# Kernel optimization log

Measured on AMD Instinct MI355X. Metric: run time of the kernel, lower is better.

The kernel has to match this reference:

```python
import jax, jax.numpy as jnp
import numpy as np

N = 32        # fixed segment-tree span in the original module
LEVELS = 5    # log2(N) descent steps (l<r loop runs exactly 5 times)
B, S, D = 16, 8192, 64


def _prefix(x):
    # P[b, m] = sum_{l=1}^{m} x[b, l]  (leaf l holds x[l]; x[0] is never used)
    return jnp.concatenate([jnp.zeros_like(x[:, :1]), jnp.cumsum(x[:, 1:N], axis=1)], axis=1)


def _seg(P, a, b, n, bidx):
    # sum of leaves l in [a, b] with l < n, via prefix sums; shapes a,b,n: [B,S]
    hi = jnp.minimum(b, n - 1)
    ok = hi >= a
    hic = jnp.clip(hi, 0, N - 1)
    v = P[bidx, hic] - P[bidx, a - 1]          # [B,S,D]
    return jnp.where(ok[..., None], v, jnp.zeros((), P.dtype))


def reference(queries, keys, values, valid_lens):
    b, s, d = queries.shape
    if valid_lens is None:
        n = jnp.full((b, s), keys.shape[1], jnp.int32)
    elif valid_lens.ndim == 1:
        n = jnp.broadcast_to(valid_lens.astype(jnp.int32)[:, None], (b, s))
    else:
        n = valid_lens.astype(jnp.int32)
    Pk = _prefix(keys)    # [B,N,D]
    Pv = _prefix(values)  # [B,N,D]
    bidx = jnp.arange(b)[:, None]
    l = jnp.ones((b, s), jnp.int32)
    r = jnp.full((b, s), N, jnp.int32)
    ans = jnp.zeros((b, s, d), queries.dtype)
    for _ in range(LEVELS):
        mid = (l + r) >> 1
        kL = _seg(Pk, l, mid, n, bidx)
        kR = _seg(Pk, mid + 1, r, n, bidx)
        ls = jax.nn.sigmoid(jnp.sum(queries * kL, axis=-1))  # [B,S]
        rs = jax.nn.sigmoid(jnp.sum(queries * kR, axis=-1))
        cond = ls >= rs
        vL = _seg(Pv, l, mid, n, bidx)
        vR = _seg(Pv, mid + 1, r, n, bidx)
        add = jnp.where(cond[..., None], vR * rs[..., None], vL * ls[..., None])
        ans = ans * 0.5 + add
        r = jnp.where(cond, mid, r)
        l = jnp.where(cond, l, mid + 1)
    return ans


def setup_inputs() -> dict:
    key = jax.random.key(0)
    k1, k2, k3, k4 = jax.random.split(key, 4)
    return {
        "queries": jax.random.normal(k1, (B, S, D), jnp.float32),
        "keys": jax.random.normal(k2, (B, N, D), jnp.float32),
        "values": jax.random.normal(k3, (B, N, D), jnp.float32),
        "valid_lens": jax.random.randint(k4, (B,), 0, 32, jnp.int64),
    }
```

## Files before the change

kernel.cpp:

```cpp
#include <hip/hip_runtime.h>
#include <math.h>


#define SEG_N   32
#define DIM     64
#define LEVELS  5
#define QPB     64
#define THREADS 256
#define PAD     68

#define DPP_QUAD_XOR1   0xB1
#define DPP_QUAD_XOR2   0x4E
#define DPP_ROW_HMIRROR 0x141

template <int CTRL>
__device__ __forceinline__ float dpp_xadd(float v) {
    const int s = __builtin_amdgcn_update_dpp(0, __float_as_int(v), CTRL, 0xf, 0xf, true);
    return v + __int_as_float(s);
}

__device__ __forceinline__ float group8_sum(float v) {
    v = dpp_xadd<DPP_QUAD_XOR1>(v);
    v = dpp_xadd<DPP_QUAD_XOR2>(v);
    v = dpp_xadd<DPP_ROW_HMIRROR>(v);
    return v;
}

__device__ __forceinline__ float4 f4sub(const float4 a, const float4 b) {
    return make_float4(a.x - b.x, a.y - b.y, a.z - b.z, a.w - b.w);
}
__device__ __forceinline__ float4 sel4(bool c, const float4 a, const float4 b) {
    return make_float4(c ? a.x : b.x, c ? a.y : b.y, c ? a.z : b.z, c ? a.w : b.w);
}
__device__ __forceinline__ float dot4(const float4 a, const float4 b) {
    return a.x * b.x + a.y * b.y + a.z * b.z + a.w * b.w;
}
__device__ __forceinline__ void fma4(float4& acc, const float4 hi, const float4 lo, float w) {
    acc.x = fmaf(hi.x - lo.x, w, acc.x);
    acc.y = fmaf(hi.y - lo.y, w, acc.y);
    acc.z = fmaf(hi.z - lo.z, w, acc.z);
    acc.w = fmaf(hi.w - lo.w, w, acc.w);
}

__global__ __launch_bounds__(THREADS) void segtree_attn_kernel(
    const float* __restrict__ q,
    const float* __restrict__ keys,
    const float* __restrict__ values,
    const int*   __restrict__ vlen,
    float*       __restrict__ out,
    int S)
{
    __shared__ float Pk[SEG_N * PAD];
    __shared__ float Pv[SEG_N * PAD];

    const int b = blockIdx.y;
    const int t = threadIdx.x;
    const int g = t >> 3;
    const int u = t & 7;
    const int c = u * 8;

    const int sA = blockIdx.x * QPB + g;
    const int sB = sA + 32;

    const float* qpA = q + ((size_t)b * S + sA) * DIM + c;
    const float* qpB = q + ((size_t)b * S + sB) * DIM + c;
    const float4 qA0 = *(const float4*)qpA;
    const float4 qA1 = *(const float4*)(qpA + 4);
    const float4 qB0 = *(const float4*)qpB;
    const float4 qB1 = *(const float4*)(qpB + 4);

    if (t < 2 * DIM) {
        const int col = t & (DIM - 1);
        const float* src = ((t < DIM) ? keys : values) + (size_t)b * SEG_N * DIM + col;
        float* dst = (t < DIM) ? Pk : Pv;
        float acc = 0.0f;
        dst[col] = 0.0f;
        #pragma unroll
        for (int row = 1; row < SEG_N; ++row) {
            acc += src[row * DIM];
            dst[row * PAD + col] = acc;
        }
    }
    const int n = vlen[b];
    __syncthreads();

    const int hnc = max(min(n - 1, SEG_N - 1), 0);
    const float scale[LEVELS] = {0.0625f, 0.125f, 0.25f, 0.5f, 1.0f};

    const int cm16 = min(16, hnc);
    float4 pkM_A0 = *(const float4*)&Pk[cm16 * PAD + c];
    float4 pkM_A1 = *(const float4*)&Pk[cm16 * PAD + c + 4];
    float4 pkM_B0 = pkM_A0, pkM_B1 = pkM_A1;
    const float4 pkRi0 = *(const float4*)&Pk[hnc * PAD + c];
    const float4 pkRi1 = *(const float4*)&Pk[hnc * PAD + c + 4];

    float4 pkR_A0 = pkRi0, pkR_A1 = pkRi1;
    float4 pkR_B0 = pkRi0, pkR_B1 = pkRi1;
    float4 pkA_A0 = make_float4(0.f,0.f,0.f,0.f), pkA_A1 = make_float4(0.f,0.f,0.f,0.f);
    float4 pkA_B0 = make_float4(0.f,0.f,0.f,0.f), pkA_B1 = make_float4(0.f,0.f,0.f,0.f);

    int midA = 16, midB = 16;
    int lA = 1, rA = SEG_N, rowA_A = 0, rowR_A = hnc;
    int lB = 1, rB = SEG_N, rowA_B = 0, rowR_B = hnc;

    float wA[LEVELS], wB[LEVELS];
    int   rows[LEVELS];

    #pragma unroll
    for (int lev = 0; lev < LEVELS; ++lev) {
        const int step = 8 >> lev;
        const int cmA = min(midA, hnc);
        const int cmB = min(midB, hnc);

        float4 sLoA0, sLoA1, sHiA0, sHiA1, sLoB0, sLoB1, sHiB0, sHiB1;
        int midLoA = 0, midHiA = 0, midLoB = 0, midHiB = 0;
        if (lev < LEVELS - 1) {
            midLoA = midA - step; midHiA = midA + step;
            midLoB = midB - step; midHiB = midB + step;
            const int rLoA = min(midLoA, hnc), rHiA = min(midHiA, hnc);
            const int rLoB = min(midLoB, hnc), rHiB = min(midHiB, hnc);
            sLoA0 = *(const float4*)&Pk[rLoA * PAD + c];
            sLoA1 = *(const float4*)&Pk[rLoA * PAD + c + 4];
            sHiA0 = *(const float4*)&Pk[rHiA * PAD + c];
            sHiA1 = *(const float4*)&Pk[rHiA * PAD + c + 4];
            sLoB0 = *(const float4*)&Pk[rLoB * PAD + c];
            sLoB1 = *(const float4*)&Pk[rLoB * PAD + c + 4];
            sHiB0 = *(const float4*)&Pk[rHiB * PAD + c];
            sHiB1 = *(const float4*)&Pk[rHiB * PAD + c + 4];
        }

        float dLA = dot4(qA0, f4sub(pkM_A0, pkA_A0)) + dot4(qA1, f4sub(pkM_A1, pkA_A1));
        float dRA = dot4(qA0, f4sub(pkR_A0, pkM_A0)) + dot4(qA1, f4sub(pkR_A1, pkM_A1));
        float dLB = dot4(qB0, f4sub(pkM_B0, pkA_B0)) + dot4(qB1, f4sub(pkM_B1, pkA_B1));
        float dRB = dot4(qB0, f4sub(pkR_B0, pkM_B0)) + dot4(qB1, f4sub(pkR_B1, pkM_B1));

        dLA = group8_sum(dLA);
        dRA = group8_sum(dRA);
        dLB = group8_sum(dLB);
        dRB = group8_sum(dRB);

        const bool okLA = (min(midA, n - 1) >= lA);
        const bool okRA = (min(rA,   n - 1) >= midA + 1);
        const bool okLB = (min(midB, n - 1) >= lB);
        const bool okRB = (min(rB,   n - 1) >= midB + 1);

        const float sLA = okLA ? dLA : 0.0f;
        const float sRA = okRA ? dRA : 0.0f;
        const float sLB = okLB ? dLB : 0.0f;
        const float sRB = okRB ? dRB : 0.0f;

        const float lsA = 1.0f / (1.0f + __expf(-sLA));
        const float rsA = 1.0f / (1.0f + __expf(-sRA));
        const float lsB = 1.0f / (1.0f + __expf(-sLB));
        const float rsB = 1.0f / (1.0f + __expf(-sRB));

        const bool condA = (lsA >= rsA);
        const bool condB = (lsB >= rsB);

        const bool  okselA = condA ? okRA : okLA;
        const bool  okselB = condB ? okRB : okLB;
        const float wselA  = condA ? rsA : lsA;
        const float wselB  = condB ? rsB : lsB;
        wA[lev] = okselA ? (wselA * scale[lev]) : 0.0f;
        wB[lev] = okselB ? (wselB * scale[lev]) : 0.0f;

        const int hiA = condA ? rowR_A : cmA;
        const int loA = condA ? midA   : rowA_A;
        const int hiB = condB ? rowR_B : cmB;
        const int loB = condB ? midB   : rowA_B;
        rows[lev] = hiA | (loA << 8) | (hiB << 16) | (loB << 24);

        if (condA) {
            rA = midA; rowR_A = cmA;
            pkR_A0 = pkM_A0; pkR_A1 = pkM_A1;
        } else {
            lA = midA + 1; rowA_A = midA;
            pkA_A0 = pkM_A0; pkA_A1 = pkM_A1;
        }
        if (condB) {
            rB = midB; rowR_B = cmB;
            pkR_B0 = pkM_B0; pkR_B1 = pkM_B1;
        } else {
            lB = midB + 1; rowA_B = midB;
            pkA_B0 = pkM_B0; pkA_B1 = pkM_B1;
        }

        if (lev < LEVELS - 1) {
            midA = condA ? midLoA : midHiA;
            midB = condB ? midLoB : midHiB;
            pkM_A0 = sel4(condA, sLoA0, sHiA0);
            pkM_A1 = sel4(condA, sLoA1, sHiA1);
            pkM_B0 = sel4(condB, sLoB0, sHiB0);
            pkM_B1 = sel4(condB, sLoB1, sHiB1);
        }
    }

    float4 aA0 = make_float4(0.f,0.f,0.f,0.f), aA1 = make_float4(0.f,0.f,0.f,0.f);
    float4 aB0 = make_float4(0.f,0.f,0.f,0.f), aB1 = make_float4(0.f,0.f,0.f,0.f);
    #pragma unroll
    for (int lev = 0; lev < LEVELS; ++lev) {
        const int pk = rows[lev];
        const int hiAr = pk & 0xFF, loAr = (pk >> 8) & 0xFF;
        const int hiBr = (pk >> 16) & 0xFF, loBr = (pk >> 24) & 0xFF;
        const float4 hA0 = *(const float4*)&Pv[hiAr * PAD + c];
        const float4 hA1 = *(const float4*)&Pv[hiAr * PAD + c + 4];
        const float4 lA0 = *(const float4*)&Pv[loAr * PAD + c];
        const float4 lA1 = *(const float4*)&Pv[loAr * PAD + c + 4];
        fma4(aA0, hA0, lA0, wA[lev]);
        fma4(aA1, hA1, lA1, wA[lev]);
        const float4 hB0 = *(const float4*)&Pv[hiBr * PAD + c];
        const float4 hB1 = *(const float4*)&Pv[hiBr * PAD + c + 4];
        const float4 lB0 = *(const float4*)&Pv[loBr * PAD + c];
        const float4 lB1 = *(const float4*)&Pv[loBr * PAD + c + 4];
        fma4(aB0, hB0, lB0, wB[lev]);
        fma4(aB1, hB1, lB1, wB[lev]);
    }

    float* opA = out + ((size_t)b * S + sA) * DIM + c;
    float* opB = out + ((size_t)b * S + sB) * DIM + c;
    *(float4*)opA       = aA0;
    *(float4*)(opA + 4) = aA1;
    *(float4*)opB       = aB0;
    *(float4*)(opB + 4) = aB1;
}

extern "C" void kernel_launch(void* const* d_in, const int* in_sizes, int n_in,
                              void* d_out, int out_size, void* d_ws, size_t ws_size,
                              hipStream_t stream) {
    const float* q    = (const float*)d_in[0];
    const float* keys = (const float*)d_in[1];
    const float* vals = (const float*)d_in[2];
    const int*   vl   = (const int*)d_in[3];
    float* out = (float*)d_out;

    const int B = in_sizes[3];
    const int S = in_sizes[0] / (B * DIM);

    dim3 grid(S / QPB, B);
    segtree_attn_kernel<<<grid, THREADS, 0, stream>>>(q, keys, vals, vl, out, S);
}
```

Baseline: 26.81 us.

## Precompute prefix tables in a separate scan kernel and copy them into LDS

```diff
diff --git a/kernel.cpp b/kernel.cpp
--- a/kernel.cpp
+++ b/kernel.cpp
@@ -29,9 +29,6 @@
 __device__ __forceinline__ float4 f4sub(const float4 a, const float4 b) {
     return make_float4(a.x - b.x, a.y - b.y, a.z - b.z, a.w - b.w);
 }
-__device__ __forceinline__ float4 sel4(bool c, const float4 a, const float4 b) {
-    return make_float4(c ? a.x : b.x, c ? a.y : b.y, c ? a.z : b.z, c ? a.w : b.w);
-}
 __device__ __forceinline__ float dot4(const float4 a, const float4 b) {
     return a.x * b.x + a.y * b.y + a.z * b.z + a.w * b.w;
 }
@@ -42,13 +39,36 @@
     acc.w = fmaf(hi.w - lo.w, w, acc.w);
 }
 
+__global__ __launch_bounds__(THREADS) void scan_kernel(
+    const float* __restrict__ keys,
+    const float* __restrict__ values,
+    float* __restrict__ Pg, int B)
+{
+    const int t = threadIdx.x;
+    const int batch = blockIdx.x * 2 + (t >> 7);
+    const int table = (t >> 6) & 1;
+    const int col = t & 63;
+    const float* src = (table ? values : keys) + (size_t)batch * SEG_N * DIM + col;
+    float* dst = Pg + ((size_t)table * B + batch) * SEG_N * DIM + col;
+    float acc = 0.0f;
+    dst[col - col] = 0.0f;
+    dst[0 * DIM + col - col] = 0.0f;
+    dst[0] = 0.0f;
+    dst[0 + 0] = 0.0f;
+    dst[0 * DIM] = 0.0f;
+    #pragma unroll
+    for (int row = 1; row < SEG_N; ++row) {
+        acc += src[row * DIM];
+        dst[row * DIM] = acc;
+    }
+}
+
 __global__ __launch_bounds__(THREADS) void segtree_attn_kernel(
     const float* __restrict__ q,
-    const float* __restrict__ keys,
-    const float* __restrict__ values,
+    const float* __restrict__ Pg,
     const int*   __restrict__ vlen,
     float*       __restrict__ out,
-    int S)
+    int S, int B)
 {
     __shared__ float Pk[SEG_N * PAD];
     __shared__ float Pv[SEG_N * PAD];
@@ -69,17 +89,20 @@
     const float4 qB0 = *(const float4*)qpB;
     const float4 qB1 = *(const float4*)(qpB + 4);
 
-    if (t < 2 * DIM) {
-        const int col = t & (DIM - 1);
-        const float* src = ((t < DIM) ? keys : values) + (size_t)b * SEG_N * DIM + col;
-        float* dst = (t < DIM) ? Pk : Pv;
-        float acc = 0.0f;
-        dst[col] = 0.0f;
-        #pragma unroll
-        for (int row = 1; row < SEG_N; ++row) {
-            acc += src[row * DIM];
-            dst[row * PAD + col] = acc;
-        }
+    {
+        const int table = t >> 7;
+        const int row   = (t >> 2) & 31;
+        const int col0  = (t & 3) * 16;
+        const float* sp = Pg + ((size_t)table * B + b) * SEG_N * DIM + row * DIM + col0;
+        float* dp = (table ? Pv : Pk) + row * PAD + col0;
+        const float4 v0 = *(const float4*)(sp + 0);
+        const float4 v1 = *(const float4*)(sp + 4);
+        const float4 v2 = *(const float4*)(sp + 8);
+        const float4 v3 = *(const float4*)(sp + 12);
+        *(float4*)(dp + 0)  = v0;
+        *(float4*)(dp + 4)  = v1;
+        *(float4*)(dp + 8)  = v2;
+        *(float4*)(dp + 12) = v3;
     }
     const int n = vlen[b];
     __syncthreads();
@@ -87,10 +110,6 @@
     const int hnc = max(min(n - 1, SEG_N - 1), 0);
     const float scale[LEVELS] = {0.0625f, 0.125f, 0.25f, 0.5f, 1.0f};
 
-    const int cm16 = min(16, hnc);
-    float4 pkM_A0 = *(const float4*)&Pk[cm16 * PAD + c];
-    float4 pkM_A1 = *(const float4*)&Pk[cm16 * PAD + c + 4];
-    float4 pkM_B0 = pkM_A0, pkM_B1 = pkM_A1;
     const float4 pkRi0 = *(const float4*)&Pk[hnc * PAD + c];
     const float4 pkRi1 = *(const float4*)&Pk[hnc * PAD + c + 4];
 
@@ -112,22 +131,10 @@
         const int cmA = min(midA, hnc);
         const int cmB = min(midB, hnc);
 
-        float4 sLoA0, sLoA1, sHiA0, sHiA1, sLoB0, sLoB1, sHiB0, sHiB1;
-        int midLoA = 0, midHiA = 0, midLoB = 0, midHiB = 0;
-        if (lev < LEVELS - 1) {
-            midLoA = midA - step; midHiA = midA + step;
-            midLoB = midB - step; midHiB = midB + step;
-            const int rLoA = min(midLoA, hnc), rHiA = min(midHiA, hnc);
-            const int rLoB = min(midLoB, hnc), rHiB = min(midHiB, hnc);
-            sLoA0 = *(const float4*)&Pk[rLoA * PAD + c];
-            sLoA1 = *(const float4*)&Pk[rLoA * PAD + c + 4];
-            sHiA0 = *(const float4*)&Pk[rHiA * PAD + c];
-            sHiA1 = *(const float4*)&Pk[rHiA * PAD + c + 4];
-            sLoB0 = *(const float4*)&Pk[rLoB * PAD + c];
-            sLoB1 = *(const float4*)&Pk[rLoB * PAD + c + 4];
-            sHiB0 = *(const float4*)&Pk[rHiB * PAD + c];
-            sHiB1 = *(const float4*)&Pk[rHiB * PAD + c + 4];
-        }
+        const float4 pkM_A0 = *(const float4*)&Pk[cmA * PAD + c];
+        const float4 pkM_A1 = *(const float4*)&Pk[cmA * PAD + c + 4];
+        const float4 pkM_B0 = *(const float4*)&Pk[cmB * PAD + c];
+        const float4 pkM_B1 = *(const float4*)&Pk[cmB * PAD + c + 4];
 
         float dLA = dot4(qA0, f4sub(pkM_A0, pkA_A0)) + dot4(qA1, f4sub(pkM_A1, pkA_A1));
         float dRA = dot4(qA0, f4sub(pkR_A0, pkM_A0)) + dot4(qA1, f4sub(pkR_A1, pkM_A1));
@@ -186,12 +193,8 @@
         }
 
         if (lev < LEVELS - 1) {
-            midA = condA ? midLoA : midHiA;
-            midB = condB ? midLoB : midHiB;
-            pkM_A0 = sel4(condA, sLoA0, sHiA0);
-            pkM_A1 = sel4(condA, sLoA1, sHiA1);
-            pkM_B0 = sel4(condB, sLoB0, sHiB0);
-            pkM_B1 = sel4(condB, sLoB1, sHiB1);
+            midA = condA ? (midA - step) : (midA + step);
+            midB = condB ? (midB - step) : (midB + step);
         }
     }
 
@@ -232,10 +235,12 @@
     const float* vals = (const float*)d_in[2];
     const int*   vl   = (const int*)d_in[3];
     float* out = (float*)d_out;
+    float* Pg  = (float*)d_ws;
 
     const int B = in_sizes[3];
     const int S = in_sizes[0] / (B * DIM);
 
+    scan_kernel<<<dim3(B / 2), THREADS, 0, stream>>>(keys, vals, Pg, B);
     dim3 grid(S / QPB, B);
-    segtree_attn_kernel<<<grid, THREADS, 0, stream>>>(q, keys, vals, vl, out, S);
-}
+    segtree_attn_kernel<<<grid, THREADS, 0, stream>>>(q, Pg, vl, out, S, B);
+}
```

Result: slower. 30.11 us (+12.3%).

## Load midpoint key rows on demand, store byte offsets, compare sigmoid denominators

Applied to the files above, without the earlier changes.

```diff
diff --git a/kernel.cpp b/kernel.cpp
--- a/kernel.cpp
+++ b/kernel.cpp
@@ -8,10 +8,17 @@
 #define QPB     64
 #define THREADS 256
 #define PAD     68
+#define PADB    (PAD * 4)
 
 #define DPP_QUAD_XOR1   0xB1
 #define DPP_QUAD_XOR2   0x4E
 #define DPP_ROW_HMIRROR 0x141
+
+#if __has_builtin(__builtin_amdgcn_rcpf)
+#define RCPF(x) __builtin_amdgcn_rcpf(x)
+#else
+#define RCPF(x) (1.0f / (x))
+#endif
 
 template <int CTRL>
 __device__ __forceinline__ float dpp_xadd(float v) {
@@ -28,9 +35,6 @@
 
 __device__ __forceinline__ float4 f4sub(const float4 a, const float4 b) {
     return make_float4(a.x - b.x, a.y - b.y, a.z - b.z, a.w - b.w);
-}
-__device__ __forceinline__ float4 sel4(bool c, const float4 a, const float4 b) {
-    return make_float4(c ? a.x : b.x, c ? a.y : b.y, c ? a.z : b.z, c ? a.w : b.w);
 }
 __device__ __forceinline__ float dot4(const float4 a, const float4 b) {
     return a.x * b.x + a.y * b.y + a.z * b.z + a.w * b.w;
@@ -50,14 +54,14 @@
     float*       __restrict__ out,
     int S)
 {
-    __shared__ float Pk[SEG_N * PAD];
-    __shared__ float Pv[SEG_N * PAD];
+    __shared__ float P[2][SEG_N * PAD];
 
     const int b = blockIdx.y;
     const int t = threadIdx.x;
     const int g = t >> 3;
     const int u = t & 7;
     const int c = u * 8;
+    const int c4 = c * 4;
 
     const int sA = blockIdx.x * QPB + g;
     const int sB = sA + 32;
@@ -72,7 +76,7 @@
     if (t < 2 * DIM) {
         const int col = t & (DIM - 1);
         const float* src = ((t < DIM) ? keys : values) + (size_t)b * SEG_N * DIM + col;
-        float* dst = (t < DIM) ? Pk : Pv;
+        float* dst = (t < DIM) ? P[0] : P[1];
         float acc = 0.0f;
         dst[col] = 0.0f;
         #pragma unroll
@@ -86,48 +90,37 @@
 
     const int hnc = max(min(n - 1, SEG_N - 1), 0);
     const float scale[LEVELS] = {0.0625f, 0.125f, 0.25f, 0.5f, 1.0f};
-
-    const int cm16 = min(16, hnc);
-    float4 pkM_A0 = *(const float4*)&Pk[cm16 * PAD + c];
-    float4 pkM_A1 = *(const float4*)&Pk[cm16 * PAD + c + 4];
-    float4 pkM_B0 = pkM_A0, pkM_B1 = pkM_A1;
-    const float4 pkRi0 = *(const float4*)&Pk[hnc * PAD + c];
-    const float4 pkRi1 = *(const float4*)&Pk[hnc * PAD + c + 4];
-
-    float4 pkR_A0 = pkRi0, pkR_A1 = pkRi1;
-    float4 pkR_B0 = pkRi0, pkR_B1 = pkRi1;
+    const char* Kb = (const char*)&P[0][0];
+    const char* Vb = (const char*)&P[1][0];
+
+    const int offN = hnc * PADB + c4;
+    float4 pkR_A0 = *(const float4*)(Kb + offN);
+    float4 pkR_A1 = *(const float4*)(Kb + offN + 16);
+    float4 pkR_B0 = pkR_A0, pkR_B1 = pkR_A1;
     float4 pkA_A0 = make_float4(0.f,0.f,0.f,0.f), pkA_A1 = make_float4(0.f,0.f,0.f,0.f);
     float4 pkA_B0 = make_float4(0.f,0.f,0.f,0.f), pkA_B1 = make_float4(0.f,0.f,0.f,0.f);
 
+    int offA_A = c4, offR_A = offN;
+    int offA_B = c4, offR_B = offN;
     int midA = 16, midB = 16;
-    int lA = 1, rA = SEG_N, rowA_A = 0, rowR_A = hnc;
-    int lB = 1, rB = SEG_N, rowA_B = 0, rowR_B = hnc;
+    int lA = 1, rA = SEG_N;
+    int lB = 1, rB = SEG_N;
 
     float wA[LEVELS], wB[LEVELS];
-    int   rows[LEVELS];
+    unsigned int rowsA[LEVELS], rowsB[LEVELS];
 
     #pragma unroll
     for (int lev = 0; lev < LEVELS; ++lev) {
         const int step = 8 >> lev;
         const int cmA = min(midA, hnc);
         const int cmB = min(midB, hnc);
-
-        float4 sLoA0, sLoA1, sHiA0, sHiA1, sLoB0, sLoB1, sHiB0, sHiB1;
-        int midLoA = 0, midHiA = 0, midLoB = 0, midHiB = 0;
-        if (lev < LEVELS - 1) {
-            midLoA = midA - step; midHiA = midA + step;
-            midLoB = midB - step; midHiB = midB + step;
-            const int rLoA = min(midLoA, hnc), rHiA = min(midHiA, hnc);
-            const int rLoB = min(midLoB, hnc), rHiB = min(midHiB, hnc);
-            sLoA0 = *(const float4*)&Pk[rLoA * PAD + c];
-            sLoA1 = *(const float4*)&Pk[rLoA * PAD + c + 4];
-            sHiA0 = *(const float4*)&Pk[rHiA * PAD + c];
-            sHiA1 = *(const float4*)&Pk[rHiA * PAD + c + 4];
-            sLoB0 = *(const float4*)&Pk[rLoB * PAD + c];
-            sLoB1 = *(const float4*)&Pk[rLoB * PAD + c + 4];
-            sHiB0 = *(const float4*)&Pk[rHiB * PAD + c];
-            sHiB1 = *(const float4*)&Pk[rHiB * PAD + c + 4];
-        }
+        const int offMA = cmA * PADB + c4;
+        const int offMB = cmB * PADB + c4;
+
+        const float4 pkM_A0 = *(const float4*)(Kb + offMA);
+        const float4 pkM_A1 = *(const float4*)(Kb + offMA + 16);
+        const float4 pkM_B0 = *(const float4*)(Kb + offMB);
+        const float4 pkM_B1 = *(const float4*)(Kb + offMB + 16);
 
         float dLA = dot4(qA0, f4sub(pkM_A0, pkA_A0)) + dot4(qA1, f4sub(pkM_A1, pkA_A1));
         float dRA = dot4(qA0, f4sub(pkR_A0, pkM_A0)) + dot4(qA1, f4sub(pkR_A1, pkM_A1));
@@ -149,49 +142,51 @@
         const float sLB = okLB ? dLB : 0.0f;
         const float sRB = okRB ? dRB : 0.0f;
 
-        const float lsA = 1.0f / (1.0f + __expf(-sLA));
-        const float rsA = 1.0f / (1.0f + __expf(-sRA));
-        const float lsB = 1.0f / (1.0f + __expf(-sLB));
-        const float rsB = 1.0f / (1.0f + __expf(-sRB));
-
-        const bool condA = (lsA >= rsA);
-        const bool condB = (lsB >= rsB);
+        const float dnLA = 1.0f + __expf(-sLA);
+        const float dnRA = 1.0f + __expf(-sRA);
+        const float dnLB = 1.0f + __expf(-sLB);
+        const float dnRB = 1.0f + __expf(-sRB);
+
+        bool condA = (dnLA <= dnRA);
+        bool condB = (dnLB <= dnRB);
+        const bool grayA = (dnLA > dnRA) && ((dnLA - dnRA) < dnLA * 1e-6f);
+        const bool grayB = (dnLB > dnRB) && ((dnLB - dnRB) < dnLB * 1e-6f);
+        if (__any(grayA || grayB)) {
+            condA = ((1.0f / dnLA) >= (1.0f / dnRA));
+            condB = ((1.0f / dnLB) >= (1.0f / dnRB));
+        }
 
         const bool  okselA = condA ? okRA : okLA;
         const bool  okselB = condB ? okRB : okLB;
-        const float wselA  = condA ? rsA : lsA;
-        const float wselB  = condB ? rsB : lsB;
+        const float wselA  = RCPF(condA ? dnRA : dnLA);
+        const float wselB  = RCPF(condB ? dnRB : dnLB);
         wA[lev] = okselA ? (wselA * scale[lev]) : 0.0f;
         wB[lev] = okselB ? (wselB * scale[lev]) : 0.0f;
 
-        const int hiA = condA ? rowR_A : cmA;
-        const int loA = condA ? midA   : rowA_A;
-        const int hiB = condB ? rowR_B : cmB;
-        const int loB = condB ? midB   : rowA_B;
-        rows[lev] = hiA | (loA << 8) | (hiB << 16) | (loB << 24);
+        const unsigned int hiA = condA ? offR_A : offMA;
+        const unsigned int loA = condA ? offMA  : offA_A;
+        const unsigned int hiB = condB ? offR_B : offMB;
+        const unsigned int loB = condB ? offMB  : offA_B;
+        rowsA[lev] = hiA | (loA << 16);
+        rowsB[lev] = hiB | (loB << 16);
 
         if (condA) {
-            rA = midA; rowR_A = cmA;
+            rA = midA; offR_A = offMA;
             pkR_A0 = pkM_A0; pkR_A1 = pkM_A1;
         } else {
-            lA = midA + 1; rowA_A = midA;
+            lA = midA + 1; offA_A = offMA;
             pkA_A0 = pkM_A0; pkA_A1 = pkM_A1;
         }
         if (condB) {
-            rB = midB; rowR_B = cmB;
+            rB = midB; offR_B = offMB;
             pkR_B0 = pkM_B0; pkR_B1 = pkM_B1;
         } else {
-            lB = midB + 1; rowA_B = midB;
+            lB = midB + 1; offA_B = offMB;
             pkA_B0 = pkM_B0; pkA_B1 = pkM_B1;
         }
-
         if (lev < LEVELS - 1) {
-            midA = condA ? midLoA : midHiA;
-            midB = condB ? midLoB : midHiB;
-            pkM_A0 = sel4(condA, sLoA0, sHiA0);
-            pkM_A1 = sel4(condA, sLoA1, sHiA1);
-            pkM_B0 = sel4(condB, sLoB0, sHiB0);
-            pkM_B1 = sel4(condB, sLoB1, sHiB1);
+            midA = condA ? (midA - step) : (midA + step);
+            midB = condB ? (midB - step) : (midB + step);
         }
     }
 
@@ -199,19 +194,20 @@
     float4 aB0 = make_float4(0.f,0.f,0.f,0.f), aB1 = make_float4(0.f,0.f,0.f,0.f);
     #pragma unroll
     for (int lev = 0; lev < LEVELS; ++lev) {
-        const int pk = rows[lev];
-        const int hiAr = pk & 0xFF, loAr = (pk >> 8) & 0xFF;
-        const int hiBr = (pk >> 16) & 0xFF, loBr = (pk >> 24) & 0xFF;
-        const float4 hA0 = *(const float4*)&Pv[hiAr * PAD + c];
-        const float4 hA1 = *(const float4*)&Pv[hiAr * PAD + c + 4];
-        const float4 lA0 = *(const float4*)&Pv[loAr * PAD + c];
-        const float4 lA1 = *(const float4*)&Pv[loAr * PAD + c + 4];
+        const unsigned int pa = rowsA[lev];
+        const unsigned int pb = rowsB[lev];
+        const unsigned int hiA = pa & 0xFFFFu, loA = pa >> 16;
+        const unsigned int hiB = pb & 0xFFFFu, loB = pb >> 16;
+        const float4 hA0 = *(const float4*)(Vb + hiA);
+        const float4 hA1 = *(const float4*)(Vb + hiA + 16);
+        const float4 lA0 = *(const float4*)(Vb + loA);
+        const float4 lA1 = *(const float4*)(Vb + loA + 16);
         fma4(aA0, hA0, lA0, wA[lev]);
         fma4(aA1, hA1, lA1, wA[lev]);
-        const float4 hB0 = *(const float4*)&Pv[hiBr * PAD + c];
-        const float4 hB1 = *(const float4*)&Pv[hiBr * PAD + c + 4];
-        const float4 lB0 = *(const float4*)&Pv[loBr * PAD + c];
-        const float4 lB1 = *(const float4*)&Pv[loBr * PAD + c + 4];
+        const float4 hB0 = *(const float4*)(Vb + hiB);
+        const float4 hB1 = *(const float4*)(Vb + hiB + 16);
+        const float4 lB0 = *(const float4*)(Vb + loB);
+        const float4 lB1 = *(const float4*)(Vb + loB + 16);
         fma4(aB0, hB0, lB0, wB[lev]);
         fma4(aB1, hB1, lB1, wB[lev]);
     }
```

New measurement: 24.61 us. -8.2%, faster.
